# Optimization experiments

Hardware: AMD Instinct MI355X
Metric: run time of the kernel (lower is better)

Reference implementation:

```python
import jax, jax.numpy as jnp
import numpy as np

N, LQ, LK = 16, 1024, 1024
DQ = DK = DE = DP = 512          # head_dim_q, head_dim_k, embed_d, proj_d
DA = DE + DQ                      # attention output width (1024)
D2 = DE + 2 * DQ                  # transformer-block width after second concat (1536)
EPS = 1e-5


def layernorm(x, g, b):
    mu = jnp.mean(x, axis=-1, keepdims=True)
    var = jnp.var(x, axis=-1, keepdims=True)
    return (x - mu) * jax.lax.rsqrt(var + EPS) * g + b


def setup_inputs() -> dict:
    root = jax.random.key(0)
    ks = jax.random.split(root, 12)
    s = 0.02
    return {
        "value": jax.random.normal(ks[0], (N, LK, DK), jnp.float32),
        "key": jax.random.normal(ks[1], (N, LK, DK), jnp.float32),
        "query": jax.random.normal(ks[2], (N, LQ, DQ), jnp.float32),
        "Wk": jax.random.normal(ks[3], (DK, DP), jnp.float32) * s,
        "Wq": jax.random.normal(ks[4], (DQ, DP), jnp.float32) * s,
        "Wo": jax.random.normal(ks[5], (DK, DE), jnp.float32) * s,
        "bo": jnp.zeros((DE,), jnp.float32),
        "ga": jnp.ones((DA,), jnp.float32),
        "ba": jnp.zeros((DA,), jnp.float32),
        "g1": jnp.ones((D2,), jnp.float32),
        "b1": jnp.zeros((D2,), jnp.float32),
        "W1": jax.random.normal(ks[6], (D2, 2 * D2), jnp.float32) * s,
        "bf1": jnp.zeros((2 * D2,), jnp.float32),
        "W2": jax.random.normal(ks[7], (2 * D2, D2), jnp.float32) * s,
        "bf2": jnp.zeros((D2,), jnp.float32),
        "g2": jnp.ones((D2,), jnp.float32),
        "b2": jnp.zeros((D2,), jnp.float32),
    }


def reference(value, key, query, Wk, Wq, Wo, bo, ga, ba, g1, b1, W1, bf1, W2, bf2, g2, b2):
    # --- Attention (hand-rolled, full energy matrix as in the original) ---
    kp = jnp.einsum('nkd,dp->nkp', key, Wk)      # [n, LK, DP]
    qp = jnp.einsum('nqd,dp->nqp', query, Wq)    # [n, LQ, DP]
    energy = jnp.einsum('nqp,nkp->nqk', qp, kp)  # [n, LQ, LK]
    attn = jax.nn.softmax(energy / jnp.sqrt(jnp.float32(DP)), axis=2)
    out = jnp.einsum('nqk,nkh->nqh', attn, value)  # [n, LQ, DK]
    out = jnp.einsum('nqh,he->nqe', out, Wo) + bo  # [n, LQ, DE]
    combined = jnp.concatenate([out, query], axis=2)  # [n, LQ, DA]
    attn_out = layernorm(combined, ga, ba)
    # --- TransformerBlock tail ---
    x = jnp.concatenate([attn_out, query], axis=2)  # [n, LQ, D2]
    x = layernorm(x, g1, b1)
    h = jax.nn.relu(jnp.einsum('nqd,df->nqf', x, W1) + bf1)
    f = jnp.einsum('nqf,fd->nqd', h, W2) + bf2
    return layernorm(f, g2, b2)
```

## Files before the change

### kernel.cpp

```cpp
#include <hip/hip_runtime.h>


typedef __attribute__((ext_vector_type(8))) __bf16 bf16x8;
typedef __attribute__((ext_vector_type(4))) float f32x4;

#define DEV static __device__ __forceinline__

DEV unsigned short f2bf(float f) {
  union { float f; unsigned int u; } x; x.f = f;
  unsigned int u = x.u + 0x7fffu + ((x.u >> 16) & 1u);
  return (unsigned short)(u >> 16);
}

DEV void gll16(const void* g, void* l) {
  __builtin_amdgcn_global_load_lds(
      (const __attribute__((address_space(1))) void*)g,
      (__attribute__((address_space(3))) void*)l, 16, 0, 0);
}

#define MFMA16(a, b, c) (c) = __builtin_amdgcn_mfma_f32_16x16x32_bf16((a), (b), (c), 0, 0, 0)

template <typename CT, bool BIAS, bool RELU>
__global__ __launch_bounds__(512, 2)
void gemm256(const unsigned short* __restrict__ A,
             const unsigned short* __restrict__ Bt,
             CT* __restrict__ C, const float* __restrict__ bias,
             int M, int N, int K, int nbx, int nby,
             long long sA, long long sB, long long sC) {
  __shared__ __align__(16) unsigned short lds[65536];

  const int cpx = gridDim.x >> 3;
  const int id = blockIdx.x;
  const int swz = (id & 7) * cpx + (id >> 3);
  const int nxy = nbx * nby;
  const int bz = swz / nxy;
  const int rxy = swz - bz * nxy;
  const int by = rxy / nbx;
  const int bx = rxy - by * nbx;

  A  += (long long)bz * sA;
  Bt += (long long)bz * sB;
  C  += (long long)bz * sC;
  const int rowBase = by * 256, colBase = bx * 256;

  const int tid = threadIdx.x;
  const int w = tid >> 6, lane = tid & 63;
  const int wm = w >> 2, wn = w & 3;

  const int lr = lane >> 2;
  const int sc = (((lane & 3) ^ ((lane >> 3) & 3)) << 3);
  const long long Kll = K;
  const unsigned short* gA0 = A  + (long long)(rowBase + w * 16 + lr) * Kll + sc;
  const unsigned short* gA1 = gA0 + 128 * Kll;
  const unsigned short* gB0 = Bt + (long long)(colBase + w * 16 + lr) * Kll + sc;
  const unsigned short* gB1 = gB0 + 128 * Kll;
  char* const Lb = (char*)lds;
  const int dA0 = w * 1024, dA1 = (w + 8) * 1024;

  const int sig = (lane >> 4) ^ ((lane >> 1) & 3);
  const int aoff = (wm * 128 + (lane & 15)) * 32 + sig * 8;
  const int boff = (wn * 64 + (lane & 15)) * 32 + sig * 8;

  f32x4 acc[8][4];
#pragma unroll
  for (int m = 0; m < 8; ++m)
#pragma unroll
    for (int n = 0; n < 4; ++n) acc[m][n] = f32x4{0.f, 0.f, 0.f, 0.f};

  const int NT = K >> 5;
  const int npro = NT < 3 ? NT : 3;
  for (int p = 0; p < npro; ++p) {
    gll16(gA0 + (long long)p * 32, Lb + (p << 15) + dA0);
    gll16(gA1 + (long long)p * 32, Lb + (p << 15) + dA1);
    gll16(gB0 + (long long)p * 32, Lb + (p << 15) + 16384 + dA0);
    gll16(gB1 + (long long)p * 32, Lb + (p << 15) + 16384 + dA1);
  }
  if (NT >= 3) asm volatile("s_waitcnt vmcnt(8)" ::: "memory");
  else         asm volatile("s_waitcnt vmcnt(0)" ::: "memory");
  __builtin_amdgcn_sched_barrier(0);
  __builtin_amdgcn_s_barrier();
  __builtin_amdgcn_sched_barrier(0);

  for (int t = 0; t < NT; ++t) {
    const int slot = t & 3;
    const unsigned short* sa = lds + slot * 16384;
    const unsigned short* sb = sa + 8192;
    bf16x8 av[8];
#pragma unroll
    for (int m = 0; m < 8; ++m)
      av[m] = *(const bf16x8*)(sa + aoff + m * 512);
    bf16x8 bv0 = *(const bf16x8*)(sb + boff);
    bf16x8 bv1 = *(const bf16x8*)(sb + boff + 512);
    if (t + 3 < NT) {
      const int ss = (t + 3) & 3;
      gll16(gA0 + (long long)(t + 3) * 32, Lb + (ss << 15) + dA0);
      gll16(gA1 + (long long)(t + 3) * 32, Lb + (ss << 15) + dA1);
    }
    __builtin_amdgcn_sched_barrier(0);
    __builtin_amdgcn_s_barrier();
    __builtin_amdgcn_sched_barrier(0);
    __builtin_amdgcn_s_setprio(1);
#pragma unroll
    for (int m = 0; m < 8; ++m) {
      MFMA16(av[m], bv0, acc[m][0]);
      MFMA16(av[m], bv1, acc[m][1]);
    }
    __builtin_amdgcn_s_setprio(0);
    __builtin_amdgcn_sched_barrier(0);
    __builtin_amdgcn_s_barrier();
    bf16x8 bv2 = *(const bf16x8*)(sb + boff + 1024);
    bf16x8 bv3 = *(const bf16x8*)(sb + boff + 1536);
    if (t + 3 < NT) {
      const int ss = (t + 3) & 3;
      gll16(gB0 + (long long)(t + 3) * 32, Lb + (ss << 15) + 16384 + dA0);
      gll16(gB1 + (long long)(t + 3) * 32, Lb + (ss << 15) + 16384 + dA1);
    }
    if (t + 3 < NT)      asm volatile("s_waitcnt vmcnt(8)" ::: "memory");
    else if (t + 2 < NT) asm volatile("s_waitcnt vmcnt(4)" ::: "memory");
    else if (t + 1 < NT) asm volatile("s_waitcnt vmcnt(0)" ::: "memory");
    __builtin_amdgcn_sched_barrier(0);
    __builtin_amdgcn_s_barrier();
    __builtin_amdgcn_sched_barrier(0);
    __builtin_amdgcn_s_setprio(1);
#pragma unroll
    for (int m = 0; m < 8; ++m) {
      MFMA16(av[m], bv2, acc[m][2]);
      MFMA16(av[m], bv3, acc[m][3]);
    }
    __builtin_amdgcn_s_setprio(0);
    __builtin_amdgcn_sched_barrier(0);
    __builtin_amdgcn_s_barrier();
  }

  const int r0 = rowBase + wm * 128 + ((lane >> 4) << 2);
  const int cb = colBase + wn * 64 + (lane & 15);
#pragma unroll
  for (int n = 0; n < 4; ++n) {
    const int col = cb + n * 16;
    float bvv = 0.f;
    if constexpr (BIAS) bvv = bias[col];
#pragma unroll
    for (int m = 0; m < 8; ++m) {
#pragma unroll
      for (int r = 0; r < 4; ++r) {
        float v = acc[m][n][r] + bvv;
        if constexpr (RELU) v = v > 0.f ? v : 0.f;
        const long long idx = (long long)(r0 + m * 16 + r) * N + col;
        if constexpr (sizeof(CT) == 2) C[idx] = (CT)f2bf(v);
        else                           C[idx] = (CT)v;
      }
    }
  }
}

__global__ void transpose_cast_k(const float* __restrict__ src,
                                 unsigned short* __restrict__ dst,
                                 int R, int Ccols, long long sS, long long sD) {
  __shared__ float tile[32][33];
  src += (long long)blockIdx.z * sS;
  dst += (long long)blockIdx.z * sD;
  const int rb = blockIdx.y * 32, cb = blockIdx.x * 32;
  const int tx = threadIdx.x, ty = threadIdx.y;
#pragma unroll
  for (int k = 0; k < 4; ++k)
    tile[ty + k * 8][tx] = src[(long long)(rb + ty + k * 8) * Ccols + cb + tx];
  __syncthreads();
#pragma unroll
  for (int k = 0; k < 4; ++k)
    dst[(long long)(cb + ty + k * 8) * R + rb + tx] = f2bf(tile[tx][ty + k * 8]);
}

__global__ void cast_f32_bf16_k(const float* __restrict__ src,
                                unsigned short* __restrict__ dst, long long n4) {
  long long i = (long long)blockIdx.x * 256 + threadIdx.x;
  const long long stride = (long long)gridDim.x * 256;
  for (; i < n4; i += stride) {
    float4 v = ((const float4*)src)[i];
    ushort4 o;
    o.x = f2bf(v.x); o.y = f2bf(v.y); o.z = f2bf(v.z); o.w = f2bf(v.w);
    ((ushort4*)dst)[i] = o;
  }
}

__global__ __launch_bounds__(256)
void softmax_k(const float* __restrict__ E, unsigned short* __restrict__ P) {
  __shared__ float sm[8];
  const long long row = blockIdx.x;
  const int t = threadIdx.x, w = t >> 6, lane = t & 63;
  float4 v = ((const float4*)E)[row * 256 + t];
  const float scale = 0.044194173824159216f;
  v.x *= scale; v.y *= scale; v.z *= scale; v.w *= scale;
  float mx = fmaxf(fmaxf(v.x, v.y), fmaxf(v.z, v.w));
#pragma unroll
  for (int m = 1; m < 64; m <<= 1) mx = fmaxf(mx, __shfl_xor(mx, m));
  if (lane == 0) sm[w] = mx;
  __syncthreads();
  mx = fmaxf(fmaxf(sm[0], sm[1]), fmaxf(sm[2], sm[3]));
  float e0 = __expf(v.x - mx), e1 = __expf(v.y - mx);
  float e2 = __expf(v.z - mx), e3 = __expf(v.w - mx);
  float s = e0 + e1 + e2 + e3;
#pragma unroll
  for (int m = 1; m < 64; m <<= 1) s += __shfl_xor(s, m);
  if (lane == 0) sm[4 + w] = s;
  __syncthreads();
  s = sm[4] + sm[5] + sm[6] + sm[7];
  const float inv = 1.0f / s;
  ushort4 o;
  o.x = f2bf(e0 * inv); o.y = f2bf(e1 * inv);
  o.z = f2bf(e2 * inv); o.w = f2bf(e3 * inv);
  ((ushort4*)P)[row * 256 + t] = o;
}

DEV void breduce2(float& a, float& b, float* sm, int w, int lane) {
#pragma unroll
  for (int m = 1; m < 64; m <<= 1) { a += __shfl_xor(a, m); b += __shfl_xor(b, m); }
  if (lane == 0) { sm[w] = a; sm[4 + w] = b; }
  __syncthreads();
  a = sm[0] + sm[1] + sm[2] + sm[3];
  b = sm[4] + sm[5] + sm[6] + sm[7];
  __syncthreads();
}

__global__ __launch_bounds__(256)
void ln_concat_k(const float* __restrict__ out2, const float* __restrict__ query,
                 const float* __restrict__ ga, const float* __restrict__ ba,
                 const float* __restrict__ g1, const float* __restrict__ b1,
                 unsigned short* __restrict__ xln) {
  __shared__ float sm[8];
  const long long row = blockIdx.x;
  const int t = threadIdx.x, w = t >> 6, lane = t & 63;
  const float* o = out2 + row * 512;
  const float* q = query + row * 512;
  float c0 = o[t], c1 = o[t + 256], c2 = q[t], c3 = q[t + 256];
  float s = c0 + c1 + c2 + c3;
  float ss = c0 * c0 + c1 * c1 + c2 * c2 + c3 * c3;
  breduce2(s, ss, sm, w, lane);
  float mu = s * (1.0f / 1024.0f);
  float var = ss * (1.0f / 1024.0f) - mu * mu;
  float rs = rsqrtf(var + 1e-5f);
  float a0 = (c0 - mu) * rs * ga[t] + ba[t];
  float a1 = (c1 - mu) * rs * ga[t + 256] + ba[t + 256];
  float a2 = (c2 - mu) * rs * ga[t + 512] + ba[t + 512];
  float a3 = (c3 - mu) * rs * ga[t + 768] + ba[t + 768];
  float s2 = a0 + a1 + a2 + a3 + c2 + c3;
  float ss2 = a0*a0 + a1*a1 + a2*a2 + a3*a3 + c2*c2 + c3*c3;
  breduce2(s2, ss2, sm, w, lane);
  float mu2 = s2 * (1.0f / 1536.0f);
  float var2 = ss2 * (1.0f / 1536.0f) - mu2 * mu2;
  float rs2 = rsqrtf(var2 + 1e-5f);
  unsigned short* xr = xln + row * 1536;
  xr[t]        = f2bf((a0 - mu2) * rs2 * g1[t] + b1[t]);
  xr[t + 256]  = f2bf((a1 - mu2) * rs2 * g1[t + 256] + b1[t + 256]);
  xr[t + 512]  = f2bf((a2 - mu2) * rs2 * g1[t + 512] + b1[t + 512]);
  xr[t + 768]  = f2bf((a3 - mu2) * rs2 * g1[t + 768] + b1[t + 768]);
  xr[t + 1024] = f2bf((c2 - mu2) * rs2 * g1[t + 1024] + b1[t + 1024]);
  xr[t + 1280] = f2bf((c3 - mu2) * rs2 * g1[t + 1280] + b1[t + 1280]);
}

__global__ __launch_bounds__(256)
void ln_final_k(const float* __restrict__ f, const float* __restrict__ g2,
                const float* __restrict__ b2, float* __restrict__ out) {
  __shared__ float sm[8];
  const long long row = blockIdx.x;
  const int t = threadIdx.x, w = t >> 6, lane = t & 63;
  const float* fr = f + row * 1536;
  float v[6];
  float s = 0.f, ss = 0.f;
#pragma unroll
  for (int j = 0; j < 6; ++j) { v[j] = fr[t + j * 256]; s += v[j]; ss += v[j] * v[j]; }
  breduce2(s, ss, sm, w, lane);
  float mu = s * (1.0f / 1536.0f);
  float var = ss * (1.0f / 1536.0f) - mu * mu;
  float rs = rsqrtf(var + 1e-5f);
  float* orow = out + row * 1536;
#pragma unroll
  for (int j = 0; j < 6; ++j)
    orow[t + j * 256] = (v[j] - mu) * rs * g2[t + j * 256] + b2[t + j * 256];
}

extern "C" void kernel_launch(void* const* d_in, const int* in_sizes, int n_in,
                              void* d_out, int out_size, void* d_ws, size_t ws_size,
                              hipStream_t stream) {
  const float* value = (const float*)d_in[0];
  const float* key   = (const float*)d_in[1];
  const float* query = (const float*)d_in[2];
  const float* Wk  = (const float*)d_in[3];
  const float* Wq  = (const float*)d_in[4];
  const float* Wo  = (const float*)d_in[5];
  const float* bo  = (const float*)d_in[6];
  const float* ga  = (const float*)d_in[7];
  const float* ba  = (const float*)d_in[8];
  const float* g1  = (const float*)d_in[9];
  const float* b1  = (const float*)d_in[10];
  const float* W1  = (const float*)d_in[11];
  const float* bf1 = (const float*)d_in[12];
  const float* W2  = (const float*)d_in[13];
  const float* bf2 = (const float*)d_in[14];
  const float* g2  = (const float*)d_in[15];
  const float* b2  = (const float*)d_in[16];
  float* out = (float*)d_out;
  char* ws = (char*)d_ws;

  const size_t oW1T = 0;
  const size_t oWkT = 9437184;
  const size_t oWqT = 9961472;
  const size_t oWoT = 10485760;
  const size_t oVT  = 11010048;
  const size_t oKeyB = 27787264;
  const size_t oQryB = 44564480;
  const size_t oKp   = 61341696;
  const size_t oQp   = 78118912;
  const size_t oE    = 100663296;
  const size_t oP    = oKeyB;
  const size_t oO    = oKp;
  const size_t oOut2 = oQp;
  const size_t oXln  = 27787264;
  const size_t oH    = 100663296;
  const size_t oW2T  = 201326592;
  const size_t oF    = 0;

  unsigned short* W1T = (unsigned short*)(ws + oW1T);
  unsigned short* WkT = (unsigned short*)(ws + oWkT);
  unsigned short* WqT = (unsigned short*)(ws + oWqT);
  unsigned short* WoT = (unsigned short*)(ws + oWoT);
  unsigned short* W2T = (unsigned short*)(ws + oW2T);
  unsigned short* VT  = (unsigned short*)(ws + oVT);
  unsigned short* keyB = (unsigned short*)(ws + oKeyB);
  unsigned short* qryB = (unsigned short*)(ws + oQryB);
  unsigned short* kp  = (unsigned short*)(ws + oKp);
  unsigned short* qp  = (unsigned short*)(ws + oQp);
  float*          E   = (float*)(ws + oE);
  unsigned short* P   = (unsigned short*)(ws + oP);
  unsigned short* O   = (unsigned short*)(ws + oO);
  float*          out2 = (float*)(ws + oOut2);
  unsigned short* xln = (unsigned short*)(ws + oXln);
  unsigned short* h   = (unsigned short*)(ws + oH);
  float*          f   = (float*)(ws + oF);

  const dim3 tb(32, 8);
  transpose_cast_k<<<dim3(16, 16, 1), tb, 0, stream>>>(Wk, WkT, 512, 512, 0, 0);
  transpose_cast_k<<<dim3(16, 16, 1), tb, 0, stream>>>(Wq, WqT, 512, 512, 0, 0);
  transpose_cast_k<<<dim3(16, 16, 1), tb, 0, stream>>>(Wo, WoT, 512, 512, 0, 0);
  transpose_cast_k<<<dim3(96, 48, 1), tb, 0, stream>>>(W1, W1T, 1536, 3072, 0, 0);
  transpose_cast_k<<<dim3(48, 96, 1), tb, 0, stream>>>(W2, W2T, 3072, 1536, 0, 0);
  transpose_cast_k<<<dim3(16, 32, 16), tb, 0, stream>>>(value, VT, 1024, 512, 524288, 524288);
  cast_f32_bf16_k<<<2048, 256, 0, stream>>>(key,   keyB, 2097152);
  cast_f32_bf16_k<<<2048, 256, 0, stream>>>(query, qryB, 2097152);

  gemm256<unsigned short, false, false><<<128, 512, 0, stream>>>(
      keyB, WkT, kp, nullptr, 16384, 512, 512, 2, 64, 0, 0, 0);
  gemm256<unsigned short, false, false><<<128, 512, 0, stream>>>(
      qryB, WqT, qp, nullptr, 16384, 512, 512, 2, 64, 0, 0, 0);
  gemm256<float, false, false><<<256, 512, 0, stream>>>(
      qp, kp, E, nullptr, 1024, 1024, 512, 4, 4, 524288, 524288, 1048576);
  softmax_k<<<16384, 256, 0, stream>>>(E, P);
  gemm256<unsigned short, false, false><<<128, 512, 0, stream>>>(
      P, VT, O, nullptr, 1024, 512, 1024, 2, 4, 1048576, 524288, 524288);
  gemm256<float, true, false><<<128, 512, 0, stream>>>(
      O, WoT, out2, bo, 16384, 512, 512, 2, 64, 0, 0, 0);
  ln_concat_k<<<16384, 256, 0, stream>>>(out2, query, ga, ba, g1, b1, xln);
  gemm256<unsigned short, true, true><<<768, 512, 0, stream>>>(
      xln, W1T, h, bf1, 16384, 3072, 1536, 12, 64, 0, 0, 0);
  gemm256<float, true, false><<<384, 512, 0, stream>>>(
      h, W2T, f, bf2, 16384, 1536, 3072, 6, 64, 0, 0, 0);
  ln_final_k<<<16384, 256, 0, stream>>>(f, g2, b2, out);
}
```

Measured before the change: 771.2 us.

## Double-buffer GEMM LDS fragments in registers and batch the K/Q projections

Rewrites the GEMM main loop to use two register fragment sets. While the MFMAs for tile t run, the A/B fragments for tile t+1 are read from LDS. This cuts the loop to one barrier and one waitcnt per K-step instead of four split phases, and issues all four global-to-LDS loads together. The key and query projection GEMMs are also merged into a single batched launch through strides, which assumes keyB/qryB, WkT/WqT and kp/qp sit contiguously in the workspace. The loop now assumes NT ≥ 3 and NT even, and holding two fragment sets raises register pressure.

```diff
diff --git a/kernel.cpp b/kernel.cpp
--- a/kernel.cpp
+++ b/kernel.cpp
@@ -19,6 +19,40 @@
 }
 
 #define MFMA16(a, b, c) (c) = __builtin_amdgcn_mfma_f32_16x16x32_bf16((a), (b), (c), 0, 0, 0)
+
+#define GBODY(T, AVC, BVC, AVN, BVN)                                        \
+  {                                                                         \
+    const int tt = (T);                                                     \
+    if (tt + 1 < NT) {                                                      \
+      const unsigned short* sa_ = lds + ((tt + 1) & 3) * 16384;             \
+      const unsigned short* sb_ = sa_ + 8192;                               \
+      _Pragma("unroll")                                                     \
+      for (int m_ = 0; m_ < 8; ++m_)                                        \
+        AVN[m_] = *(const bf16x8*)(sa_ + aoff + m_ * 512);                  \
+      _Pragma("unroll")                                                     \
+      for (int n_ = 0; n_ < 4; ++n_)                                        \
+        BVN[n_] = *(const bf16x8*)(sb_ + boff + n_ * 512);                  \
+    }                                                                       \
+    if (tt + 3 < NT) {                                                      \
+      const int ss_ = (tt + 3) & 3;                                         \
+      gll16(gA0 + (long long)(tt + 3) * 32, Lb + (ss_ << 15) + dA0);        \
+      gll16(gA1 + (long long)(tt + 3) * 32, Lb + (ss_ << 15) + dA1);        \
+      gll16(gB0 + (long long)(tt + 3) * 32, Lb + (ss_ << 15) + 16384 + dA0);\
+      gll16(gB1 + (long long)(tt + 3) * 32, Lb + (ss_ << 15) + 16384 + dA1);\
+    }                                                                       \
+    _Pragma("unroll")                                                       \
+    for (int m_ = 0; m_ < 8; ++m_) {                                        \
+      MFMA16(AVC[m_], BVC[0], acc[m_][0]);                                  \
+      MFMA16(AVC[m_], BVC[1], acc[m_][1]);                                  \
+      MFMA16(AVC[m_], BVC[2], acc[m_][2]);                                  \
+      MFMA16(AVC[m_], BVC[3], acc[m_][3]);                                  \
+    }                                                                       \
+    if (tt + 3 < NT)      asm volatile("s_waitcnt vmcnt(4)" ::: "memory");  \
+    else if (tt + 2 < NT) asm volatile("s_waitcnt vmcnt(0)" ::: "memory");  \
+    __builtin_amdgcn_sched_barrier(0);                                      \
+    __builtin_amdgcn_s_barrier();                                           \
+    __builtin_amdgcn_sched_barrier(0);                                      \
+  }
 
 template <typename CT, bool BIAS, bool RELU>
 __global__ __launch_bounds__(512, 2)
@@ -68,68 +102,27 @@
     for (int n = 0; n < 4; ++n) acc[m][n] = f32x4{0.f, 0.f, 0.f, 0.f};
 
   const int NT = K >> 5;
-  const int npro = NT < 3 ? NT : 3;
-  for (int p = 0; p < npro; ++p) {
+
+  for (int p = 0; p < 3; ++p) {
     gll16(gA0 + (long long)p * 32, Lb + (p << 15) + dA0);
     gll16(gA1 + (long long)p * 32, Lb + (p << 15) + dA1);
     gll16(gB0 + (long long)p * 32, Lb + (p << 15) + 16384 + dA0);
     gll16(gB1 + (long long)p * 32, Lb + (p << 15) + 16384 + dA1);
   }
-  if (NT >= 3) asm volatile("s_waitcnt vmcnt(8)" ::: "memory");
-  else         asm volatile("s_waitcnt vmcnt(0)" ::: "memory");
+  asm volatile("s_waitcnt vmcnt(4)" ::: "memory");
   __builtin_amdgcn_sched_barrier(0);
   __builtin_amdgcn_s_barrier();
   __builtin_amdgcn_sched_barrier(0);
 
-  for (int t = 0; t < NT; ++t) {
-    const int slot = t & 3;
-    const unsigned short* sa = lds + slot * 16384;
-    const unsigned short* sb = sa + 8192;
-    bf16x8 av[8];
-#pragma unroll
-    for (int m = 0; m < 8; ++m)
-      av[m] = *(const bf16x8*)(sa + aoff + m * 512);
-    bf16x8 bv0 = *(const bf16x8*)(sb + boff);
-    bf16x8 bv1 = *(const bf16x8*)(sb + boff + 512);
-    if (t + 3 < NT) {
-      const int ss = (t + 3) & 3;
-      gll16(gA0 + (long long)(t + 3) * 32, Lb + (ss << 15) + dA0);
-      gll16(gA1 + (long long)(t + 3) * 32, Lb + (ss << 15) + dA1);
-    }
-    __builtin_amdgcn_sched_barrier(0);
-    __builtin_amdgcn_s_barrier();
-    __builtin_amdgcn_sched_barrier(0);
-    __builtin_amdgcn_s_setprio(1);
-#pragma unroll
-    for (int m = 0; m < 8; ++m) {
-      MFMA16(av[m], bv0, acc[m][0]);
-      MFMA16(av[m], bv1, acc[m][1]);
-    }
-    __builtin_amdgcn_s_setprio(0);
-    __builtin_amdgcn_sched_barrier(0);
-    __builtin_amdgcn_s_barrier();
-    bf16x8 bv2 = *(const bf16x8*)(sb + boff + 1024);
-    bf16x8 bv3 = *(const bf16x8*)(sb + boff + 1536);
-    if (t + 3 < NT) {
-      const int ss = (t + 3) & 3;
-      gll16(gB0 + (long long)(t + 3) * 32, Lb + (ss << 15) + 16384 + dA0);
-      gll16(gB1 + (long long)(t + 3) * 32, Lb + (ss << 15) + 16384 + dA1);
-    }
-    if (t + 3 < NT)      asm volatile("s_waitcnt vmcnt(8)" ::: "memory");
-    else if (t + 2 < NT) asm volatile("s_waitcnt vmcnt(4)" ::: "memory");
-    else if (t + 1 < NT) asm volatile("s_waitcnt vmcnt(0)" ::: "memory");
-    __builtin_amdgcn_sched_barrier(0);
-    __builtin_amdgcn_s_barrier();
-    __builtin_amdgcn_sched_barrier(0);
-    __builtin_amdgcn_s_setprio(1);
-#pragma unroll
-    for (int m = 0; m < 8; ++m) {
-      MFMA16(av[m], bv2, acc[m][2]);
-      MFMA16(av[m], bv3, acc[m][3]);
-    }
-    __builtin_amdgcn_s_setprio(0);
-    __builtin_amdgcn_sched_barrier(0);
-    __builtin_amdgcn_s_barrier();
+  bf16x8 avA[8], bvA[4], avB[8], bvB[4];
+#pragma unroll
+  for (int m = 0; m < 8; ++m) avA[m] = *(const bf16x8*)(lds + aoff + m * 512);
+#pragma unroll
+  for (int n = 0; n < 4; ++n) bvA[n] = *(const bf16x8*)(lds + 8192 + boff + n * 512);
+
+  for (int t = 0; t < NT; t += 2) {
+    GBODY(t,     avA, bvA, avB, bvB);
+    GBODY(t + 1, avB, bvB, avA, bvA);
   }
 
   const int r0 = rowBase + wm * 128 + ((lane >> 4) << 2);
@@ -347,10 +340,8 @@
   cast_f32_bf16_k<<<2048, 256, 0, stream>>>(key,   keyB, 2097152);
   cast_f32_bf16_k<<<2048, 256, 0, stream>>>(query, qryB, 2097152);
 
-  gemm256<unsigned short, false, false><<<128, 512, 0, stream>>>(
-      keyB, WkT, kp, nullptr, 16384, 512, 512, 2, 64, 0, 0, 0);
-  gemm256<unsigned short, false, false><<<128, 512, 0, stream>>>(
-      qryB, WqT, qp, nullptr, 16384, 512, 512, 2, 64, 0, 0, 0);
+  gemm256<unsigned short, false, false><<<256, 512, 0, stream>>>(
+      keyB, WkT, kp, nullptr, 16384, 512, 512, 2, 64, 8388608, 262144, 8388608);
   gemm256<float, false, false><<<256, 512, 0, stream>>>(
       qp, kp, E, nullptr, 1024, 1024, 512, 4, 4, 524288, 524288, 1048576);
   softmax_k<<<16384, 256, 0, stream>>>(E, P);
```

After: 758.9 us. Within noise of the previous version (-1.6%).
